# Performance work log

Measured on AMD Instinct MI355X. Metric: run time of the kernel, lower is better.

## Reference

```python
import jax, jax.numpy as jnp
import numpy as np

EMBED = 1024
HEADS = 16
DH = EMBED // HEADS
B, S = 2, 2048


def setup_inputs() -> dict:
    key = jax.random.key(0)
    ks = jax.random.split(key, 12)
    inp = {
        "k": jax.random.normal(ks[0], (B, S, EMBED), jnp.float32),
        "q": jax.random.normal(ks[1], (B, S, EMBED), jnp.float32),
        "v": jax.random.normal(ks[2], (B, S, EMBED), jnp.float32),
        "mask": jax.random.randint(ks[3], (B, 1, S, S), 0, 2, jnp.int32),
        # per-head projections (shared across heads, as in the torch module)
        "Wk": jax.random.normal(ks[4], (DH, DH), jnp.float32) / np.sqrt(DH),
        "bk": jnp.zeros((DH,), jnp.float32),
        "Wq": jax.random.normal(ks[5], (DH, DH), jnp.float32) / np.sqrt(DH),
        "bq": jnp.zeros((DH,), jnp.float32),
        "Wv": jax.random.normal(ks[6], (DH, DH), jnp.float32) / np.sqrt(DH),
        "bv": jnp.zeros((DH,), jnp.float32),
        "Wo": jax.random.normal(ks[7], (EMBED, EMBED), jnp.float32) / np.sqrt(EMBED),
        "bo": jnp.zeros((EMBED,), jnp.float32),
    }
    return inp


def reference(k, q, v, mask, Wk, bk, Wq, bq, Wv, bv, Wo, bo):
    b, s, _ = k.shape
    sq = q.shape[1]
    # [B,S,H,dh]
    kh = k.reshape(b, s, HEADS, DH)
    qh = q.reshape(b, sq, HEADS, DH)
    vh = v.reshape(b, s, HEADS, DH)
    # per-head linear (weight shared across heads): x @ W.T + b
    kh = kh @ Wk.T + bk
    qh = qh @ Wq.T + bq
    vh = vh @ Wv.T + bv
    # scores [B,H,Sq,Sk]
    product = jnp.einsum("bqhd,bkhd->bhqk", qh, kh)
    # masked_fill BEFORE scaling, as in the original
    product = jnp.where(mask == 0, jnp.float32(-1e20), product)
    product = product / np.sqrt(DH)
    scores = jax.nn.softmax(product, axis=-1)
    ctx = jnp.einsum("bhqk,bkhd->bqhd", scores, vh).reshape(b, sq, EMBED)
    return ctx @ Wo.T + bo
```

## Files before the change

kernel.cpp:

```cpp
#include <hip/hip_runtime.h>
#include <hip/hip_bf16.h>
#include <math.h>

#define EMBED 1024
#define HEADS 16
#define DH    64
#define BATCH 2
#define SEQ   2048

typedef __attribute__((ext_vector_type(8))) short bf16x8;
typedef __attribute__((ext_vector_type(4))) short bf16x4;
typedef __attribute__((ext_vector_type(4))) float f32x4;
typedef unsigned long long u64;

#define QSCALE 0.1803368801111244f

static __device__ __forceinline__ unsigned short f2bf(float x) {
    unsigned u = __builtin_bit_cast(unsigned, x);
    return (unsigned short)((u + 0x7fffu + ((u >> 16) & 1u)) >> 16);
}
static __device__ __forceinline__ unsigned pk2bf(float a, float b) {
    union { __hip_bfloat162 h2; unsigned u; } c;
    c.h2 = __float22bfloat162_rn(make_float2(a, b));
    return c.u;
}
static __device__ __forceinline__ void gl_lds16(const void* g, void* l) {
    __builtin_amdgcn_global_load_lds(
        (const __attribute__((address_space(1))) void*)g,
        (__attribute__((address_space(3))) void*)l, 16, 0, 0);
}

__global__ __launch_bounds__(256) void proj_mfma(
    const float* __restrict__ q, const float* __restrict__ k, const float* __restrict__ v,
    const float* __restrict__ Wq, const float* __restrict__ bq,
    const float* __restrict__ Wk, const float* __restrict__ bk,
    const float* __restrict__ Wv, const float* __restrict__ bv,
    unsigned short* __restrict__ qh, unsigned short* __restrict__ kh,
    unsigned short* __restrict__ vh)
{
    const int blk = blockIdx.x;
    const int which = blockIdx.y;
    const float* x; const float* W; const float* bias; unsigned short* out;
    if (which == 0)      { x = q; W = Wq; bias = bq; out = qh; }
    else if (which == 1) { x = k; W = Wk; bias = bk; out = kh; }
    else                 { x = v; W = Wv; bias = bv; out = vh; }
    const float oscale = (which == 0) ? QSCALE : 1.0f;

    __shared__ unsigned short Xs[64 * 72];
    __shared__ unsigned short Ws[64 * 72];

    const int t  = threadIdx.x;
    const int sr = t >> 2, sp = t & 3;

    {
        const float* xsrc = x + ((size_t)blk * 64 + sr) * 64 + sp * 16;
        unsigned o32[8];
#pragma unroll
        for (int u4 = 0; u4 < 4; ++u4) {
            float4 a = ((const float4*)xsrc)[u4];
            o32[u4 * 2 + 0] = pk2bf(a.x, a.y);
            o32[u4 * 2 + 1] = pk2bf(a.z, a.w);
        }
        *(uint4*)&Xs[sr * 72 + sp * 16]     = *(uint4*)&o32[0];
        *(uint4*)&Xs[sr * 72 + sp * 16 + 8] = *(uint4*)&o32[4];
        const float* wsrc = W + (size_t)sr * 64 + sp * 16;
#pragma unroll
        for (int u4 = 0; u4 < 4; ++u4) {
            float4 a = ((const float4*)wsrc)[u4];
            o32[u4 * 2 + 0] = pk2bf(a.x, a.y);
            o32[u4 * 2 + 1] = pk2bf(a.z, a.w);
        }
        *(uint4*)&Ws[sr * 72 + sp * 16]     = *(uint4*)&o32[0];
        *(uint4*)&Ws[sr * 72 + sp * 16 + 8] = *(uint4*)&o32[4];
    }
    __syncthreads();

    const int w    = t >> 6;
    const int lane = t & 63;
    const int l15  = lane & 15;
    const int quad = lane >> 4;

    bf16x8 af0 = *(const bf16x8*)&Xs[(w * 16 + l15) * 72 + quad * 8];
    bf16x8 af1 = *(const bf16x8*)&Xs[(w * 16 + l15) * 72 + 32 + quad * 8];

    f32x4 acc[4];
#pragma unroll
    for (int nt = 0; nt < 4; ++nt) {
        bf16x8 bf0 = *(const bf16x8*)&Ws[(nt * 16 + l15) * 72 + quad * 8];
        bf16x8 bf1 = *(const bf16x8*)&Ws[(nt * 16 + l15) * 72 + 32 + quad * 8];
        f32x4 a = {0, 0, 0, 0};
        a = __builtin_amdgcn_mfma_f32_16x16x32_bf16(af0, bf0, a, 0, 0, 0);
        a = __builtin_amdgcn_mfma_f32_16x16x32_bf16(af1, bf1, a, 0, 0, 0);
        acc[nt] = a;
    }

    const int bsidx = blk * 4 + w;
    const int b = bsidx >> 11, s = bsidx & 2047;
#pragma unroll
    for (int nt = 0; nt < 4; ++nt) {
        const int d = nt * 16 + l15;
        const float bb = bias[d];
#pragma unroll
        for (int r = 0; r < 4; ++r) {
            const int h = quad * 4 + r;
            out[(((size_t)b * HEADS + h) * SEQ + s) * DH + d] =
                f2bf((acc[nt][r] + bb) * oscale);
        }
    }
}

__global__ __launch_bounds__(256) void prep_kernel(
    const unsigned short* __restrict__ vh, unsigned short* __restrict__ vt,
    const int* __restrict__ mask, u64* __restrict__ bits,
    const float* __restrict__ Wo, unsigned short* __restrict__ Wob)
{
    __shared__ unsigned short Tt[64 * 72];
    const int bid = blockIdx.x;
    const int t   = threadIdx.x;

    if (bid < 1024) {
        const int st = bid & 31;
        const int bh = bid >> 5;
        const int r = t >> 2, p = t & 3;
        const unsigned short* src = vh + ((size_t)bh * SEQ + st * 64 + r) * DH + p * 16;
        *(uint4*)&Tt[r * 72 + p * 16]     = *(const uint4*)src;
        *(uint4*)&Tt[r * 72 + p * 16 + 8] = *(const uint4*)(src + 8);
        __syncthreads();
        union { unsigned short u[16]; uint4 v[2]; } o;
#pragma unroll
        for (int u = 0; u < 16; ++u) o.u[u] = Tt[(p * 16 + u) * 72 + r];
        unsigned short* dst = vt + ((size_t)bh * DH + r) * SEQ + st * 64 + p * 16;
        *(uint4*)dst       = o.v[0];
        *(uint4*)(dst + 8) = o.v[1];
    } else if (bid < 1536) {
        const int idx = (bid - 1024) * 256 + t;
        const int4* src = (const int4*)(mask + (size_t)idx * 64);
        u64 w = 0;
#pragma unroll
        for (int u = 0; u < 16; ++u) {
            int4 m = src[u];
            u64 nib = (m.x != 0 ? 1ull : 0) | (m.y != 0 ? 2ull : 0) |
                      (m.z != 0 ? 4ull : 0) | (m.w != 0 ? 8ull : 0);
            w |= nib << (u * 4);
        }
        bits[idx] = w;
    } else {
        const int i = ((bid - 1536) * 256 + t) * 8;
        float4 a = ((const float4*)(Wo + i))[0];
        float4 b = ((const float4*)(Wo + i))[1];
        unsigned o32[4] = {pk2bf(a.x, a.y), pk2bf(a.z, a.w),
                           pk2bf(b.x, b.y), pk2bf(b.z, b.w)};
        *(uint4*)(Wob + i) = *(uint4*)o32;
    }
}

__global__ __launch_bounds__(256, 2) void attn_kernel(
    const unsigned short* __restrict__ qh, const unsigned short* __restrict__ kh,
    const unsigned short* __restrict__ vt, const u64* __restrict__ mbits,
    unsigned short* __restrict__ ctx)
{
    const int bid = blockIdx.x;
    const int bh  = bid & 31;
    const int q0  = (bid >> 5) * 64;
    const int b   = bh >> 4;

    __shared__ unsigned char smem[65536];

    const int t    = threadIdx.x;
    const int hh   = t >> 7;
    const int w2   = (t >> 6) & 1;
    const int lane = t & 63;
    const int l15  = lane & 15;
    const int quad = lane >> 4;

    const int srow   = lane >> 3;
    const int schunk = (lane & 7) ^ srow;

    bf16x8 qf[2][2];
#pragma unroll
    for (int g = 0; g < 2; ++g) {
        const unsigned short* qb =
            qh + ((size_t)bh * SEQ + q0 + w2 * 32 + g * 16 + l15) * DH + quad * 8;
        qf[g][0] = *(const bf16x8*)qb;
        qf[g][1] = *(const bf16x8*)(qb + 32);
    }

    f32x4 O[2][4];
#pragma unroll
    for (int g = 0; g < 2; ++g)
#pragma unroll
        for (int dt = 0; dt < 4; ++dt) O[g][dt] = f32x4{0, 0, 0, 0};
    f32x4 Osum[2] = {f32x4{0, 0, 0, 0}, f32x4{0, 0, 0, 0}};
    const bf16x4 ones = {(short)0x3F80, (short)0x3F80, (short)0x3F80, (short)0x3F80};

    const unsigned short* kbase = kh + (size_t)bh * SEQ * DH + (size_t)hh * 1024 * DH
                                  + (size_t)srow * DH + schunk * 8;
    const unsigned short* vbase = vt + (size_t)bh * DH * SEQ + hh * 1024
                                  + (size_t)srow * SEQ + schunk * 8;
    const u64* mrow0 = mbits + ((size_t)b * SEQ + q0 + w2 * 32 + l15) * (SEQ / 64) + hh * 16;
    const u64* mrow1 = mrow0 + 16 * (SEQ / 64);

    if (w2 == 0) {
        unsigned char* Kd = smem + hh * 16384;
#pragma unroll
        for (int i = 0; i < 8; ++i)
            gl_lds16(kbase + (size_t)i * 8 * DH, Kd + i * 1024);
    } else {
        unsigned char* Vd = smem + hh * 16384 + 8192;
#pragma unroll
        for (int i = 0; i < 8; ++i)
            gl_lds16(vbase + (size_t)i * 8 * SEQ, Vd + i * 1024);
    }
    u64 pm0 = mrow0[0], pm1 = mrow1[0];
    __syncthreads();

    for (int kt = 0; kt < 16; ++kt) {
        if (kt < 15) {
            const int bn = (kt + 1) & 1;
            if (w2 == 0) {
                unsigned char* Kd = smem + bn * 32768 + hh * 16384;
                const unsigned short* g0 = kbase + (size_t)(kt + 1) * 64 * DH;
#pragma unroll
                for (int i = 0; i < 8; ++i)
                    gl_lds16(g0 + (size_t)i * 8 * DH, Kd + i * 1024);
            } else {
                unsigned char* Vd = smem + bn * 32768 + hh * 16384 + 8192;
                const unsigned short* g0 = vbase + (kt + 1) * 64;
#pragma unroll
                for (int i = 0; i < 8; ++i)
                    gl_lds16(g0 + (size_t)i * 8 * SEQ, Vd + i * 1024);
            }
        }
        const u64 mb0 = pm0, mb1 = pm1;
        if (kt < 15) { pm0 = mrow0[kt + 1]; pm1 = mrow1[kt + 1]; }

        const unsigned short* KtH = (const unsigned short*)(smem + (kt & 1) * 32768 + hh * 16384);
        const unsigned short* VtH = KtH + 4096;

        bf16x4 p[2][4];
        const int rx = l15 & 7;
#pragma unroll
        for (int st = 0; st < 4; ++st) {
            const int r = st * 16 + l15;
            bf16x8 kf0 = *(const bf16x8*)&KtH[r * 64 + ((quad ^ rx)) * 8];
            bf16x8 kf1 = *(const bf16x8*)&KtH[r * 64 + ((quad ^ rx) ^ 4) * 8];
#pragma unroll
            for (int g = 0; g < 2; ++g) {
                f32x4 sa = {0, 0, 0, 0};
                sa = __builtin_amdgcn_mfma_f32_16x16x32_bf16(kf0, qf[g][0], sa, 0, 0, 0);
                sa = __builtin_amdgcn_mfma_f32_16x16x32_bf16(kf1, qf[g][1], sa, 0, 0, 0);
                const unsigned nib = (unsigned)((g ? mb1 : mb0) >> (st * 16 + quad * 4)) & 0xFu;
                float p0 = (nib & 1u) ? exp2f(sa[0]) : 0.f;
                float p1 = (nib & 2u) ? exp2f(sa[1]) : 0.f;
                float p2 = (nib & 4u) ? exp2f(sa[2]) : 0.f;
                float p3 = (nib & 8u) ? exp2f(sa[3]) : 0.f;
                union { unsigned u2[2]; bf16x4 v; } pu;
                pu.u2[0] = pk2bf(p0, p1);
                pu.u2[1] = pk2bf(p2, p3);
                p[g][st] = pu.v;
                Osum[g] = __builtin_amdgcn_mfma_f32_16x16x16bf16_1k(p[g][st], ones, Osum[g], 0, 0, 0);
            }
        }

#pragma unroll
        for (int dt = 0; dt < 4; ++dt) {
            const int d = dt * 16 + l15;
            const int dx = l15 & 7;
#pragma unroll
            for (int st = 0; st < 4; ++st) {
                const int ch = (st * 2 + (quad >> 1)) ^ dx;
                bf16x4 vb = *(const bf16x4*)&VtH[d * 64 + ch * 8 + (quad & 1) * 4];
                O[0][dt] = __builtin_amdgcn_mfma_f32_16x16x16bf16_1k(p[0][st], vb, O[0][dt], 0, 0, 0);
                O[1][dt] = __builtin_amdgcn_mfma_f32_16x16x16bf16_1k(p[1][st], vb, O[1][dt], 0, 0, 0);
            }
        }
        __syncthreads();
    }

    float* Obuf = (float*)smem;
    float* Ls   = ((float*)smem) + 64 * 68;

    if (hh == 0) {
#pragma unroll
        for (int g = 0; g < 2; ++g) {
#pragma unroll
            for (int dt = 0; dt < 4; ++dt)
#pragma unroll
                for (int r = 0; r < 4; ++r)
                    Obuf[(w2 * 32 + g * 16 + quad * 4 + r) * 68 + dt * 16 + l15] = O[g][dt][r];
            if (l15 == 0) {
#pragma unroll
                for (int r = 0; r < 4; ++r)
                    Ls[w2 * 32 + g * 16 + quad * 4 + r] = Osum[g][r];
            }
        }
    }
    __syncthreads();
    if (hh == 1) {
#pragma unroll
        for (int g = 0; g < 2; ++g) {
            float invr[4];
#pragma unroll
            for (int r = 0; r < 4; ++r) {
                const int row = w2 * 32 + g * 16 + quad * 4 + r;
                invr[r] = 1.0f / (Osum[g][r] + Ls[row]);
            }
#pragma unroll
            for (int r = 0; r < 4; ++r) {
                const int row = w2 * 32 + g * 16 + quad * 4 + r;
                unsigned short* dst = ctx + ((size_t)bh * SEQ + q0 + row) * DH + l15;
#pragma unroll
                for (int dt = 0; dt < 4; ++dt) {
                    const float val = O[g][dt][r] + Obuf[row * 68 + dt * 16 + l15];
                    dst[dt * 16] = f2bf(val * invr[r]);
                }
            }
        }
    }
}

__global__ __launch_bounds__(256, 4) void outproj_mfma(
    const unsigned short* __restrict__ ctx, const unsigned short* __restrict__ Wob,
    const float* __restrict__ bo, float* __restrict__ out)
{
    const int n0 = blockIdx.x * 64;
    const int m0 = blockIdx.y * 64;
    const int b  = m0 / SEQ;
    const int s0 = m0 % SEQ;

    __shared__ unsigned char smem[32768];

    const int t    = threadIdx.x;
    const int w    = t >> 6;
    const int lane = t & 63;
    const int l15  = lane & 15;
    const int quad = lane >> 4;
    const int srow   = lane >> 3;
    const int schunk = (lane & 7) ^ srow;

    const unsigned short* abase = ctx + ((size_t)b * HEADS * SEQ + s0 + srow) * DH + schunk * 8;
    const unsigned short* wbase = Wob + (size_t)(n0 + srow) * EMBED + schunk * 8;

    f32x4 acc[4] = {f32x4{0,0,0,0}, f32x4{0,0,0,0}, f32x4{0,0,0,0}, f32x4{0,0,0,0}};

    {
        unsigned char* Ab = smem;
        unsigned char* Wb = smem + 8192;
#pragma unroll
        for (int j = 0; j < 4; ++j) {
            const int idx = w * 4 + j;
            if (idx < 8)
                gl_lds16(abase + (size_t)idx * 8 * DH, Ab + idx * 1024);
            else
                gl_lds16(wbase + (size_t)(idx - 8) * 8 * EMBED, Wb + (idx - 8) * 1024);
        }
    }
    __syncthreads();

    for (int kt = 0; kt < 16; ++kt) {
        if (kt < 15) {
            const int ktn = kt + 1;
            unsigned char* Ab = smem + (ktn & 1) * 16384;
            unsigned char* Wb = Ab + 8192;
#pragma unroll
            for (int j = 0; j < 4; ++j) {
                const int idx = w * 4 + j;
                if (idx < 8)
                    gl_lds16(abase + (size_t)ktn * SEQ * DH + (size_t)idx * 8 * DH,
                             Ab + idx * 1024);
                else
                    gl_lds16(wbase + (size_t)(idx - 8) * 8 * EMBED + ktn * 64,
                             Wb + (idx - 8) * 1024);
            }
        }

        const unsigned short* At = (const unsigned short*)(smem + (kt & 1) * 16384);
        const unsigned short* Wt = At + 4096;
        const int rx = l15 & 7;
        const int c0 = ((quad ^ rx)) * 8;

        bf16x8 bf0 = *(const bf16x8*)&Wt[(w * 16 + l15) * 64 + c0];
        bf16x8 bf1 = *(const bf16x8*)&Wt[(w * 16 + l15) * 64 + (c0 ^ 32)];
#pragma unroll
        for (int mt = 0; mt < 4; ++mt) {
            bf16x8 af0 = *(const bf16x8*)&At[(mt * 16 + l15) * 64 + c0];
            bf16x8 af1 = *(const bf16x8*)&At[(mt * 16 + l15) * 64 + (c0 ^ 32)];
            acc[mt] = __builtin_amdgcn_mfma_f32_16x16x32_bf16(af0, bf0, acc[mt], 0, 0, 0);
            acc[mt] = __builtin_amdgcn_mfma_f32_16x16x32_bf16(af1, bf1, acc[mt], 0, 0, 0);
        }
        __syncthreads();
    }

    const float bv = bo[n0 + w * 16 + l15];
#pragma unroll
    for (int mt = 0; mt < 4; ++mt) {
#pragma unroll
        for (int r = 0; r < 4; ++r) {
            out[(size_t)(m0 + mt * 16 + quad * 4 + r) * EMBED + n0 + w * 16 + l15] =
                acc[mt][r] + bv;
        }
    }
}

extern "C" void kernel_launch(void* const* d_in, const int* in_sizes, int n_in,
                              void* d_out, int out_size, void* d_ws, size_t ws_size,
                              hipStream_t stream) {
    const float* k    = (const float*)d_in[0];
    const float* q    = (const float*)d_in[1];
    const float* v    = (const float*)d_in[2];
    const int*   mask = (const int*)  d_in[3];
    const float* Wk   = (const float*)d_in[4];
    const float* bk   = (const float*)d_in[5];
    const float* Wq   = (const float*)d_in[6];
    const float* bq   = (const float*)d_in[7];
    const float* Wv   = (const float*)d_in[8];
    const float* bv   = (const float*)d_in[9];
    const float* Wo   = (const float*)d_in[10];
    const float* bo   = (const float*)d_in[11];
    float* out = (float*)d_out;

    const size_t TEN = (size_t)BATCH * HEADS * SEQ * DH;
    unsigned short* qh_bf = (unsigned short*)d_ws;
    unsigned short* kh_bf = qh_bf + TEN;
    unsigned short* vh_bf = kh_bf + TEN;
    unsigned short* vt_bf = vh_bf + TEN;
    unsigned short* ctxb  = vt_bf + TEN;
    unsigned short* Wob   = ctxb + TEN;
    u64*            mbits = (u64*)(Wob + EMBED * EMBED);

    proj_mfma<<<dim3(BATCH * SEQ * HEADS / 64, 3), 256, 0, stream>>>(
        q, k, v, Wq, bq, Wk, bk, Wv, bv, qh_bf, kh_bf, vh_bf);
    prep_kernel<<<dim3(2048), 256, 0, stream>>>(
        vh_bf, vt_bf, mask, mbits, Wo, Wob);
    attn_kernel<<<dim3((SEQ / 64) * BATCH * HEADS), 256, 0, stream>>>(
        qh_bf, kh_bf, vt_bf, mbits, ctxb);
    outproj_mfma<<<dim3(EMBED / 64, BATCH * SEQ / 64), 256, 0, stream>>>(
        ctxb, Wob, bo, out);
}
```

Baseline: 245.2 us.

## Drop key-split across wave halves; each wave owns 16 query rows over full sequence

The attention kernel used to split the key sequence between two halves of the block, with each wave handling 32 query rows and merging partial outputs through shared memory. Now each of the four waves owns 16 query rows and walks all 32 key tiles, and all four waves cooperatively load each shared K/V tile. This halves shared memory and drops the cross-half reduction, so launch bounds can ask for 4 blocks per CU. The cost is twice as many loop iterations and barriers per block, and each K/V fragment read from LDS now feeds only one query group instead of two.

```diff
diff --git a/kernel.cpp b/kernel.cpp
--- a/kernel.cpp
+++ b/kernel.cpp
@@ -154,7 +154,7 @@
     }
 }
 
-__global__ __launch_bounds__(256, 2) void attn_kernel(
+__global__ __launch_bounds__(256, 4) void attn_kernel(
     const unsigned short* __restrict__ qh, const unsigned short* __restrict__ kh,
     const unsigned short* __restrict__ vt, const u64* __restrict__ mbits,
     unsigned short* __restrict__ ctx)
@@ -164,11 +164,10 @@
     const int q0  = (bid >> 5) * 64;
     const int b   = bh >> 4;
 
-    __shared__ unsigned char smem[65536];
+    __shared__ unsigned char smem[32768];
 
     const int t    = threadIdx.x;
-    const int hh   = t >> 7;
-    const int w2   = (t >> 6) & 1;
+    const int w    = t >> 6;
     const int lane = t & 63;
     const int l15  = lane & 15;
     const int quad = lane >> 4;
@@ -176,90 +175,88 @@
     const int srow   = lane >> 3;
     const int schunk = (lane & 7) ^ srow;
 
-    bf16x8 qf[2][2];
-#pragma unroll
-    for (int g = 0; g < 2; ++g) {
-        const unsigned short* qb =
-            qh + ((size_t)bh * SEQ + q0 + w2 * 32 + g * 16 + l15) * DH + quad * 8;
-        qf[g][0] = *(const bf16x8*)qb;
-        qf[g][1] = *(const bf16x8*)(qb + 32);
-    }
-
-    f32x4 O[2][4];
-#pragma unroll
-    for (int g = 0; g < 2; ++g)
-#pragma unroll
-        for (int dt = 0; dt < 4; ++dt) O[g][dt] = f32x4{0, 0, 0, 0};
-    f32x4 Osum[2] = {f32x4{0, 0, 0, 0}, f32x4{0, 0, 0, 0}};
+    const unsigned short* qb = qh + ((size_t)bh * SEQ + q0 + w * 16 + l15) * DH + quad * 8;
+    const bf16x8 qf0 = *(const bf16x8*)qb;
+    const bf16x8 qf1 = *(const bf16x8*)(qb + 32);
+
+    f32x4 O[4];
+#pragma unroll
+    for (int dt = 0; dt < 4; ++dt) O[dt] = f32x4{0, 0, 0, 0};
+    f32x4 Osum = {0, 0, 0, 0};
     const bf16x4 ones = {(short)0x3F80, (short)0x3F80, (short)0x3F80, (short)0x3F80};
 
-    const unsigned short* kbase = kh + (size_t)bh * SEQ * DH + (size_t)hh * 1024 * DH
+    const unsigned short* kbase = kh + (size_t)bh * SEQ * DH
                                   + (size_t)srow * DH + schunk * 8;
-    const unsigned short* vbase = vt + (size_t)bh * DH * SEQ + hh * 1024
+    const unsigned short* vbase = vt + (size_t)bh * DH * SEQ
                                   + (size_t)srow * SEQ + schunk * 8;
-    const u64* mrow0 = mbits + ((size_t)b * SEQ + q0 + w2 * 32 + l15) * (SEQ / 64) + hh * 16;
-    const u64* mrow1 = mrow0 + 16 * (SEQ / 64);
-
-    if (w2 == 0) {
-        unsigned char* Kd = smem + hh * 16384;
-#pragma unroll
-        for (int i = 0; i < 8; ++i)
+    const u64* mrow = mbits + ((size_t)b * SEQ + q0 + w * 16 + l15) * (SEQ / 64);
+
+    if (w < 2) {
+        unsigned char* Kd = smem;
+#pragma unroll
+        for (int j = 0; j < 4; ++j) {
+            const int i = w * 4 + j;
             gl_lds16(kbase + (size_t)i * 8 * DH, Kd + i * 1024);
+        }
     } else {
-        unsigned char* Vd = smem + hh * 16384 + 8192;
-#pragma unroll
-        for (int i = 0; i < 8; ++i)
+        unsigned char* Vd = smem + 8192;
+#pragma unroll
+        for (int j = 0; j < 4; ++j) {
+            const int i = (w - 2) * 4 + j;
             gl_lds16(vbase + (size_t)i * 8 * SEQ, Vd + i * 1024);
-    }
-    u64 pm0 = mrow0[0], pm1 = mrow1[0];
+        }
+    }
+    u64 pm = mrow[0];
     __syncthreads();
 
-    for (int kt = 0; kt < 16; ++kt) {
-        if (kt < 15) {
+    for (int kt = 0; kt < 32; ++kt) {
+        if (kt < 31) {
             const int bn = (kt + 1) & 1;
-            if (w2 == 0) {
-                unsigned char* Kd = smem + bn * 32768 + hh * 16384;
+            if (w < 2) {
+                unsigned char* Kd = smem + bn * 16384;
                 const unsigned short* g0 = kbase + (size_t)(kt + 1) * 64 * DH;
 #pragma unroll
-                for (int i = 0; i < 8; ++i)
+                for (int j = 0; j < 4; ++j) {
+                    const int i = w * 4 + j;
                     gl_lds16(g0 + (size_t)i * 8 * DH, Kd + i * 1024);
+                }
             } else {
-                unsigned char* Vd = smem + bn * 32768 + hh * 16384 + 8192;
+                unsigned char* Vd = smem + bn * 16384 + 8192;
                 const unsigned short* g0 = vbase + (kt + 1) * 64;
 #pragma unroll
-                for (int i = 0; i < 8; ++i)
+                for (int j = 0; j < 4; ++j) {
+                    const int i = (w - 2) * 4 + j;
                     gl_lds16(g0 + (size_t)i * 8 * SEQ, Vd + i * 1024);
+                }
             }
         }
-        const u64 mb0 = pm0, mb1 = pm1;
-        if (kt < 15) { pm0 = mrow0[kt + 1]; pm1 = mrow1[kt + 1]; }
-
-        const unsigned short* KtH = (const unsigned short*)(smem + (kt & 1) * 32768 + hh * 16384);
+        const u64 mb = pm;
+        if (kt < 31) pm = mrow[kt + 1];
+
+        const unsigned short* KtH = (const unsigned short*)(smem + (kt & 1) * 16384);
         const unsigned short* VtH = KtH + 4096;
 
-        bf16x4 p[2][4];
+        const u64 mq = mb >> (quad * 4);
+        bf16x4 p[4];
         const int rx = l15 & 7;
 #pragma unroll
         for (int st = 0; st < 4; ++st) {
             const int r = st * 16 + l15;
             bf16x8 kf0 = *(const bf16x8*)&KtH[r * 64 + ((quad ^ rx)) * 8];
             bf16x8 kf1 = *(const bf16x8*)&KtH[r * 64 + ((quad ^ rx) ^ 4) * 8];
-#pragma unroll
-            for (int g = 0; g < 2; ++g) {
-                f32x4 sa = {0, 0, 0, 0};
-                sa = __builtin_amdgcn_mfma_f32_16x16x32_bf16(kf0, qf[g][0], sa, 0, 0, 0);
-                sa = __builtin_amdgcn_mfma_f32_16x16x32_bf16(kf1, qf[g][1], sa, 0, 0, 0);
-                const unsigned nib = (unsigned)((g ? mb1 : mb0) >> (st * 16 + quad * 4)) & 0xFu;
-                float p0 = (nib & 1u) ? exp2f(sa[0]) : 0.f;
-                float p1 = (nib & 2u) ? exp2f(sa[1]) : 0.f;
-                float p2 = (nib & 4u) ? exp2f(sa[2]) : 0.f;
-                float p3 = (nib & 8u) ? exp2f(sa[3]) : 0.f;
-                union { unsigned u2[2]; bf16x4 v; } pu;
-                pu.u2[0] = pk2bf(p0, p1);
-                pu.u2[1] = pk2bf(p2, p3);
-                p[g][st] = pu.v;
-                Osum[g] = __builtin_amdgcn_mfma_f32_16x16x16bf16_1k(p[g][st], ones, Osum[g], 0, 0, 0);
-            }
+            f32x4 sa = {0, 0, 0, 0};
+            sa = __builtin_amdgcn_mfma_f32_16x16x32_bf16(kf0, qf0, sa, 0, 0, 0);
+            sa = __builtin_amdgcn_mfma_f32_16x16x32_bf16(kf1, qf1, sa, 0, 0, 0);
+            const unsigned nib = (unsigned)(mq >> (st * 16)) & 0xFu;
+            float p0 = (nib & 1u) ? exp2f(sa[0]) : 0.f;
+            float p1 = (nib & 2u) ? exp2f(sa[1]) : 0.f;
+            float p2 = (nib & 4u) ? exp2f(sa[2]) : 0.f;
+            float p3 = (nib & 8u) ? exp2f(sa[3]) : 0.f;
+            union { unsigned u2[2]; bf16x4 v; } pu;
+            pu.u2[0] = pk2bf(p0, p1);
+            pu.u2[1] = pk2bf(p2, p3);
+            p[st] = pu.v;
+            Osum = __builtin_amdgcn_mfma_f32_16x16x16bf16_1k(p[st], ones, Osum, 0, 0, 0);
         }
 
 #pragma unroll
@@ -270,52 +267,22 @@
             for (int st = 0; st < 4; ++st) {
                 const int ch = (st * 2 + (quad >> 1)) ^ dx;
                 bf16x4 vb = *(const bf16x4*)&VtH[d * 64 + ch * 8 + (quad & 1) * 4];
-                O[0][dt] = __builtin_amdgcn_mfma_f32_16x16x16bf16_1k(p[0][st], vb, O[0][dt], 0, 0, 0);
-                O[1][dt] = __builtin_amdgcn_mfma_f32_16x16x16bf16_1k(p[1][st], vb, O[1][dt], 0, 0, 0);
+                O[dt] = __builtin_amdgcn_mfma_f32_16x16x16bf16_1k(p[st], vb, O[dt], 0, 0, 0);
             }
         }
         __syncthreads();
     }
 
-    float* Obuf = (float*)smem;
-    float* Ls   = ((float*)smem) + 64 * 68;
-
-    if (hh == 0) {
-#pragma unroll
-        for (int g = 0; g < 2; ++g) {
-#pragma unroll
-            for (int dt = 0; dt < 4; ++dt)
-#pragma unroll
-                for (int r = 0; r < 4; ++r)
-                    Obuf[(w2 * 32 + g * 16 + quad * 4 + r) * 68 + dt * 16 + l15] = O[g][dt][r];
-            if (l15 == 0) {
-#pragma unroll
-                for (int r = 0; r < 4; ++r)
-                    Ls[w2 * 32 + g * 16 + quad * 4 + r] = Osum[g][r];
-            }
-        }
-    }
-    __syncthreads();
-    if (hh == 1) {
-#pragma unroll
-        for (int g = 0; g < 2; ++g) {
-            float invr[4];
-#pragma unroll
-            for (int r = 0; r < 4; ++r) {
-                const int row = w2 * 32 + g * 16 + quad * 4 + r;
-                invr[r] = 1.0f / (Osum[g][r] + Ls[row]);
-            }
-#pragma unroll
-            for (int r = 0; r < 4; ++r) {
-                const int row = w2 * 32 + g * 16 + quad * 4 + r;
-                unsigned short* dst = ctx + ((size_t)bh * SEQ + q0 + row) * DH + l15;
-#pragma unroll
-                for (int dt = 0; dt < 4; ++dt) {
-                    const float val = O[g][dt][r] + Obuf[row * 68 + dt * 16 + l15];
-                    dst[dt * 16] = f2bf(val * invr[r]);
-                }
-            }
-        }
+    float inv[4];
+#pragma unroll
+    for (int r = 0; r < 4; ++r) inv[r] = 1.0f / Osum[r];
+#pragma unroll
+    for (int r = 0; r < 4; ++r) {
+        const int row = q0 + w * 16 + quad * 4 + r;
+        unsigned short* dst = ctx + ((size_t)bh * SEQ + row) * DH + l15;
+#pragma unroll
+        for (int dt = 0; dt < 4; ++dt)
+            dst[dt * 16] = f2bf(O[dt][r] * inv[r]);
     }
 }
 
```

New measurement: 240.1 us. 1.02x faster.
